# Kernel optimization log

Hardware: AMD Instinct MI355X
Metric: run time of the kernel (lower is better)

Reference implementation:

```python
import jax, jax.numpy as jnp
import numpy as np

N_EMBD = 1024
N_HEAD = 16
HEAD_DIM = N_EMBD // N_HEAD
D_FF = 4 * N_EMBD
B, T = 2, 2048


def setup_inputs() -> dict:
    key = jax.random.key(0)
    ks = jax.random.split(key, 16)
    s = 0.02
    d = {
        'x': jax.random.normal(ks[0], (B, T, N_EMBD), jnp.float32),
        'ln1_g': jnp.ones((N_EMBD,), jnp.float32),
        'ln1_b': jnp.zeros((N_EMBD,), jnp.float32),
        'Wq': jax.random.normal(ks[1], (N_EMBD, N_EMBD), jnp.float32) * s,
        'bq': jnp.zeros((N_EMBD,), jnp.float32),
        'Wk': jax.random.normal(ks[2], (N_EMBD, N_EMBD), jnp.float32) * s,
        'bk': jnp.zeros((N_EMBD,), jnp.float32),
        'Wv': jax.random.normal(ks[3], (N_EMBD, N_EMBD), jnp.float32) * s,
        'bv': jnp.zeros((N_EMBD,), jnp.float32),
        'Wo': jax.random.normal(ks[4], (N_EMBD, N_EMBD), jnp.float32) * s,
        'bo': jnp.zeros((N_EMBD,), jnp.float32),
        'ln2_g': jnp.ones((N_EMBD,), jnp.float32),
        'ln2_b': jnp.zeros((N_EMBD,), jnp.float32),
        'W1': jax.random.normal(ks[5], (N_EMBD, D_FF), jnp.float32) * s,
        'b1': jnp.zeros((D_FF,), jnp.float32),
        'W2': jax.random.normal(ks[6], (D_FF, N_EMBD), jnp.float32) * s,
        'b2': jnp.zeros((N_EMBD,), jnp.float32),
    }
    return d


def _layernorm(x, g, b, eps=1e-5):
    mu = jnp.mean(x, axis=-1, keepdims=True)
    var = jnp.var(x, axis=-1, keepdims=True)
    return (x - mu) * jax.lax.rsqrt(var + eps) * g + b


def _attention(x, Wq, bq, Wk, bk, Wv, bv, Wo, bo):
    b, t, c = x.shape
    q = (x @ Wq + bq).reshape(b, t, N_HEAD, HEAD_DIM).transpose(0, 2, 1, 3)
    k = (x @ Wk + bk).reshape(b, t, N_HEAD, HEAD_DIM).transpose(0, 2, 1, 3)
    v = (x @ Wv + bv).reshape(b, t, N_HEAD, HEAD_DIM).transpose(0, 2, 1, 3)
    att = jnp.einsum('bhqd,bhkd->bhqk', q, k) / jnp.sqrt(jnp.float32(HEAD_DIM))
    causal = jnp.tril(jnp.ones((t, t), bool))
    att = jnp.where(causal[None, None], att, -jnp.inf)
    att = jax.nn.softmax(att, axis=-1)
    y = jnp.einsum('bhqk,bhkd->bhqd', att, v)
    y = y.transpose(0, 2, 1, 3).reshape(b, t, c)
    return y @ Wo + bo


def reference(x, ln1_g, ln1_b, Wq, bq, Wk, bk, Wv, bv, Wo, bo, ln2_g, ln2_b, W1, b1, W2, b2):
    x = x + _attention(_layernorm(x, ln1_g, ln1_b), Wq, bq, Wk, bk, Wv, bv, Wo, bo)
    h = _layernorm(x, ln2_g, ln2_b)
    h = jax.nn.gelu(h @ W1 + b1, approximate=False) @ W2 + b2
    return x + h
```

## Files before the change

### kernel.cpp

```cpp
#include <hip/hip_runtime.h>
#include <hip/hip_bf16.h>

typedef __hip_bfloat16 bf16;
using bf16x8 = __attribute__((ext_vector_type(8))) short;
using f32x4  = __attribute__((ext_vector_type(4))) float;
using f32x16 = __attribute__((ext_vector_type(16))) float;
using u32x4  = __attribute__((ext_vector_type(4))) unsigned int;

#define TSEQ 2048
#define NH   16
#define HD   64
#define NC   1024
#define DFF  4096
#define NROWS 4096

__device__ __forceinline__ float b2f(short s) {
  unsigned int u = ((unsigned int)(unsigned short)s) << 16;
  return __builtin_bit_cast(float, u);
}

__device__ __forceinline__ unsigned cvtpk(float a, float b) {
  unsigned r;
  asm("v_cvt_pk_bf16_f32 %0, %1, %2" : "=v"(r) : "v"(a), "v"(b));
  return r;
}

__device__ __forceinline__ void pl32swap(unsigned &d, unsigned &s) {
  asm("v_permlane32_swap_b32 %0, %1" : "+v"(d), "+v"(s));
}

__device__ __forceinline__ float gelu_f(float x) {
  float u = 0.7978845608028654f * fmaf(0.044715f * x, x * x, x);
  float e = __expf(2.0f * u);
  float t = 1.0f - 2.0f / (e + 1.0f);
  return 0.5f * x * (1.0f + t);
}

__global__ __launch_bounds__(256)
void ln_cast_kernel(const float* __restrict__ x, const float* __restrict__ g,
                    const float* __restrict__ b, bf16* __restrict__ out) {
  int row = blockIdx.x, tid = threadIdx.x;
  const float4 v = ((const float4*)(x + (size_t)row * NC))[tid];
  float s  = v.x + v.y + v.z + v.w;
  float s2 = v.x*v.x + v.y*v.y + v.z*v.z + v.w*v.w;
#pragma unroll
  for (int m = 1; m < 64; m <<= 1) { s += __shfl_xor(s, m); s2 += __shfl_xor(s2, m); }
  __shared__ float rs[4], rs2[4];
  if ((tid & 63) == 0) { rs[tid >> 6] = s; rs2[tid >> 6] = s2; }
  __syncthreads();
  s  = rs[0] + rs[1] + rs[2] + rs[3];
  s2 = rs2[0] + rs2[1] + rs2[2] + rs2[3];
  float mu   = s * (1.0f / NC);
  float var  = s2 * (1.0f / NC) - mu * mu;
  float rstd = rsqrtf(var + 1e-5f);
  const float4 gv = ((const float4*)g)[tid];
  const float4 bv = ((const float4*)b)[tid];
  bf16* o = out + (size_t)row * NC + tid * 4;
  o[0] = __float2bfloat16((v.x - mu) * rstd * gv.x + bv.x);
  o[1] = __float2bfloat16((v.y - mu) * rstd * gv.y + bv.y);
  o[2] = __float2bfloat16((v.z - mu) * rstd * gv.z + bv.z);
  o[3] = __float2bfloat16((v.w - mu) * rstd * gv.w + bv.w);
}

__global__ __launch_bounds__(256)
void wo_ln_kernel(const float* __restrict__ x, const float* __restrict__ bo,
                  const bf16* __restrict__ P, const float* __restrict__ g,
                  const float* __restrict__ bln, float* __restrict__ x2,
                  bf16* __restrict__ xn2) {
  int row = blockIdx.x, tid = threadIdx.x;
  size_t base = (size_t)row * NC + tid * 4;
  const float4 xv = *(const float4*)(x + base);
  const float4 bv = ((const float4*)bo)[tid];
  short4 p0 = *(const short4*)((const short*)P + base);
  short4 p1 = *(const short4*)((const short*)P + (size_t)NROWS * NC + base);
  float v0 = xv.x + bv.x + b2f(p0.x) + b2f(p1.x);
  float v1 = xv.y + bv.y + b2f(p0.y) + b2f(p1.y);
  float v2 = xv.z + bv.z + b2f(p0.z) + b2f(p1.z);
  float v3 = xv.w + bv.w + b2f(p0.w) + b2f(p1.w);
  float4 ov = {v0, v1, v2, v3};
  *(float4*)(x2 + base) = ov;
  float s  = v0 + v1 + v2 + v3;
  float s2 = v0*v0 + v1*v1 + v2*v2 + v3*v3;
#pragma unroll
  for (int m = 1; m < 64; m <<= 1) { s += __shfl_xor(s, m); s2 += __shfl_xor(s2, m); }
  __shared__ float rs[4], rs2[4];
  if ((tid & 63) == 0) { rs[tid >> 6] = s; rs2[tid >> 6] = s2; }
  __syncthreads();
  s  = rs[0] + rs[1] + rs[2] + rs[3];
  s2 = rs2[0] + rs2[1] + rs2[2] + rs2[3];
  float mu   = s * (1.0f / NC);
  float var  = s2 * (1.0f / NC) - mu * mu;
  float rstd = rsqrtf(var + 1e-5f);
  const float4 gv = ((const float4*)g)[tid];
  const float4 lv = ((const float4*)bln)[tid];
  bf16* o = xn2 + base;
  o[0] = __float2bfloat16((v0 - mu) * rstd * gv.x + lv.x);
  o[1] = __float2bfloat16((v1 - mu) * rstd * gv.y + lv.y);
  o[2] = __float2bfloat16((v2 - mu) * rstd * gv.z + lv.z);
  o[3] = __float2bfloat16((v3 - mu) * rstd * gv.w + lv.w);
}

__global__ __launch_bounds__(256)
void w2_final_kernel(const float* __restrict__ x2, const float* __restrict__ b2,
                     const bf16* __restrict__ P, float* __restrict__ out) {
  int row = blockIdx.x, tid = threadIdx.x;
  size_t base = (size_t)row * NC + tid * 4;
  const float4 xv = *(const float4*)(x2 + base);
  const float4 bv = ((const float4*)b2)[tid];
  float a0 = xv.x + bv.x, a1 = xv.y + bv.y, a2 = xv.z + bv.z, a3 = xv.w + bv.w;
#pragma unroll
  for (int z = 0; z < 4; ++z) {
    short4 p = *(const short4*)((const short*)P + (size_t)z * NROWS * NC + base);
    a0 += b2f(p.x); a1 += b2f(p.y); a2 += b2f(p.z); a3 += b2f(p.w);
  }
  float4 ov = {a0, a1, a2, a3};
  *(float4*)(out + base) = ov;
}

__global__ __launch_bounds__(256)
void transpose_all_kernel(const float* __restrict__ Wq, const float* __restrict__ Wk,
                          const float* __restrict__ Wv, const float* __restrict__ Wo,
                          const float* __restrict__ W1, const float* __restrict__ W2,
                          bf16* __restrict__ WqkvoT, bf16* __restrict__ W1T,
                          bf16* __restrict__ W2T) {
  int bid = blockIdx.x;
  const float* W; bf16* Wt; int K, N, nx, tile;
  if (bid < 4096) {
    int z = bid >> 10; tile = bid & 1023;
    W = (z == 0) ? Wq : (z == 1) ? Wk : (z == 2) ? Wv : Wo;
    Wt = WqkvoT + (size_t)z * NC * NC; K = NC; N = NC; nx = 32;
  } else if (bid < 8192) {
    tile = bid - 4096; W = W1; Wt = W1T; K = NC; N = DFF; nx = 128;
  } else {
    tile = bid - 8192; W = W2; Wt = W2T; K = DFF; N = NC; nx = 32;
  }
  int n0 = (tile % nx) * 32, k0 = (tile / nx) * 32;
  __shared__ float t[32][33];
  int tx = threadIdx.x, ty = threadIdx.y;
#pragma unroll
  for (int i = 0; i < 4; ++i)
    t[ty + i * 8][tx] = W[(size_t)(k0 + ty + i * 8) * N + n0 + tx];
  __syncthreads();
#pragma unroll
  for (int i = 0; i < 4; ++i)
    Wt[(size_t)(n0 + ty + i * 8) * K + k0 + tx] = __float2bfloat16(t[tx][ty + i * 8]);
}

#define MODE_GELU 4
#define MODE_QKV  5
#define MODE_PART 6

template <int MODE>
__global__ __launch_bounds__(512, 2)
void gemm256(const bf16* __restrict__ A, const bf16* __restrict__ Bt,
             const float* __restrict__ bias, const float* __restrict__ bias2,
             const float* __restrict__ bias3,
             void* __restrict__ outp, void* __restrict__ out2, void* __restrict__ out3,
             int M, int N, int K, int KS) {
  __shared__ bf16 lds[32768];
  int tid  = threadIdx.x;
  int w    = tid >> 6;
  int lane = tid & 63;
  int l31  = lane & 31;
  int kb   = lane >> 5;
  int wm   = w >> 2, wn = w & 3;

  int gN = gridDim.x, gM = gridDim.y;
  int pid = blockIdx.y * gN + blockIdx.x;
  int npg = 4 * gN;
  int gid = pid / npg;
  int fm  = gid * 4;
  int gsz = min(gM - fm, 4);
  int bm = (fm + (pid % gsz)) * 256;
  int bn = ((pid % npg) / gsz) * 256;
  int k_beg = blockIdx.z * KS;

  int c = lane & 3;
  int q = lane >> 2;
  const bf16* gA = A  + (size_t)(bm + w * 32 + q) * K + k_beg + c * 8;
  const bf16* gB = Bt + (size_t)(bn + w * 32 + q) * K + k_beg + c * 8;
  int wr = (w * 2 + (c >> 1)) * 512 + ((c & 1) * 32 + q) * 8;

  bf16x8 ra0, ra1, rb0, rb1;
  ra0 = *(const bf16x8*)(gA);
  ra1 = *(const bf16x8*)(gA + (size_t)16 * K);
  rb0 = *(const bf16x8*)(gB);
  rb1 = *(const bf16x8*)(gB + (size_t)16 * K);

  f32x16 acc[4][2];
#pragma unroll
  for (int mi = 0; mi < 4; ++mi)
#pragma unroll
    for (int ni = 0; ni < 2; ++ni)
#pragma unroll
      for (int r = 0; r < 16; ++r) acc[mi][ni][r] = 0.f;

  int NT = KS >> 5;
  for (int t = 0; t < NT; ++t) {
    bf16* dA = &lds[(t & 1) * 8192];
    bf16* dB = &lds[16384 + (t & 1) * 8192];
    *(bf16x8*)(dA + wr)       = ra0;
    *(bf16x8*)(dA + wr + 128) = ra1;
    *(bf16x8*)(dB + wr)       = rb0;
    *(bf16x8*)(dB + wr + 128) = rb1;
    if (t + 1 < NT) {
      size_t ko = (size_t)(t + 1) * 32;
      ra0 = *(const bf16x8*)(gA + ko);
      ra1 = *(const bf16x8*)(gA + ko + (size_t)16 * K);
      rb0 = *(const bf16x8*)(gB + ko);
      rb1 = *(const bf16x8*)(gB + ko + (size_t)16 * K);
    }
    __builtin_amdgcn_sched_barrier(0);
    asm volatile("s_waitcnt lgkmcnt(0)" ::: "memory");
    __builtin_amdgcn_s_barrier();
    __builtin_amdgcn_sched_barrier(0);

    const bf16* bufA = &lds[(t & 1) * 8192];
    const bf16* bufB = &lds[16384 + (t & 1) * 8192];
    bf16x8 af[2][4], bfr[2][2];
#pragma unroll
    for (int ks = 0; ks < 2; ++ks) {
#pragma unroll
      for (int mi = 0; mi < 4; ++mi)
        af[ks][mi] = *(const bf16x8*)&bufA[((wm * 4 + mi) * 2 + ks) * 512 + lane * 8];
#pragma unroll
      for (int ni = 0; ni < 2; ++ni)
        bfr[ks][ni] = *(const bf16x8*)&bufB[((wn * 2 + ni) * 2 + ks) * 512 + lane * 8];
    }
    __builtin_amdgcn_s_setprio(1);
#pragma unroll
    for (int ks = 0; ks < 2; ++ks)
#pragma unroll
      for (int mi = 0; mi < 4; ++mi)
#pragma unroll
        for (int ni = 0; ni < 2; ++ni)
          acc[mi][ni] = __builtin_amdgcn_mfma_f32_32x32x16_bf16(af[ks][mi], bfr[ks][ni], acc[mi][ni], 0, 0, 0);
    __builtin_amdgcn_s_setprio(0);
  }

  if (MODE == MODE_PART) {
    bf16* dst = (bf16*)outp + (size_t)blockIdx.z * M * N;
#pragma unroll
    for (int mi = 0; mi < 4; ++mi)
#pragma unroll
      for (int ni = 0; ni < 2; ++ni) {
        int col = bn + wn * 64 + ni * 32 + l31;
#pragma unroll
        for (int reg = 0; reg < 16; ++reg) {
          int row = bm + wm * 128 + mi * 32 + (reg & 3) + 8 * (reg >> 2) + 4 * kb;
          dst[(size_t)row * N + col] = __float2bfloat16(acc[mi][ni][reg]);
        }
      }
  } else if (MODE == MODE_GELU) {
    float bcol[2];
#pragma unroll
    for (int ni = 0; ni < 2; ++ni) bcol[ni] = bias[bn + wn * 64 + ni * 32 + l31];
#pragma unroll
    for (int mi = 0; mi < 4; ++mi)
#pragma unroll
      for (int ni = 0; ni < 2; ++ni) {
        int col = bn + wn * 64 + ni * 32 + l31;
#pragma unroll
        for (int reg = 0; reg < 16; ++reg) {
          int row = bm + wm * 128 + mi * 32 + (reg & 3) + 8 * (reg >> 2) + 4 * kb;
          ((bf16*)outp)[(size_t)row * N + col] =
              __float2bfloat16(gelu_f(acc[mi][ni][reg] + bcol[ni]));
        }
      }
  } else {
    int seg = bn >> 10;
    int c1b = (bn & (NC - 1)) + wn * 64;
    const float* bp = (seg == 0) ? bias : (seg == 1) ? bias2 : bias3;
    float bcol[2]; int hh[2], dd[2];
#pragma unroll
    for (int ni = 0; ni < 2; ++ni) {
      int c1 = c1b + ni * 32 + l31;
      bcol[ni] = bp[c1]; hh[ni] = c1 >> 6; dd[ni] = c1 & (HD - 1);
    }
    if (seg == 0) {
      bf16* dst = (bf16*)outp;
#pragma unroll
      for (int mi = 0; mi < 4; ++mi)
#pragma unroll
        for (int reg = 0; reg < 16; ++reg) {
          int row = bm + wm * 128 + mi * 32 + (reg & 3) + 8 * (reg >> 2) + 4 * kb;
          int bbi = row >> 11, t = row & (TSEQ - 1);
#pragma unroll
          for (int ni = 0; ni < 2; ++ni)
            dst[((size_t)(bbi * NH + hh[ni]) * TSEQ + t) * HD + dd[ni]] =
                __float2bfloat16(acc[mi][ni][reg] + bcol[ni]);
        }
    } else if (seg == 1) {
      bf16* dst = (bf16*)out2;
#pragma unroll
      for (int mi = 0; mi < 4; ++mi)
#pragma unroll
        for (int reg = 0; reg < 16; ++reg) {
          int row = bm + wm * 128 + mi * 32 + (reg & 3) + 8 * (reg >> 2) + 4 * kb;
          int bbi = row >> 11, t = row & (TSEQ - 1);
          int kt = t >> 5, lk = t & 31;
#pragma unroll
          for (int ni = 0; ni < 2; ++ni) {
            int d = dd[ni];
            size_t off = ((((size_t)(bbi * NH + hh[ni]) * 64 + kt) * 4 + (d >> 4)) * 64
                          + ((d >> 3) & 1) * 32 + lk) * 8 + (d & 7);
            dst[off] = __float2bfloat16(acc[mi][ni][reg] + bcol[ni]);
          }
        }
    } else {
      bf16* dst = (bf16*)out3;
#pragma unroll
      for (int mi = 0; mi < 4; ++mi)
#pragma unroll
        for (int reg = 0; reg < 16; ++reg) {
          int row = bm + wm * 128 + mi * 32 + (reg & 3) + 8 * (reg >> 2) + 4 * kb;
          int bbi = row >> 11, t = row & (TSEQ - 1);
          int kt = t >> 5, rem = t & 31;
          int ks = rem >> 4, hf = (rem >> 3) & 1, j = rem & 7;
#pragma unroll
          for (int ni = 0; ni < 2; ++ni) {
            int d = dd[ni];
            size_t off = (((((size_t)(bbi * NH + hh[ni]) * 64 + kt) * 2 + (d >> 5)) * 2 + ks) * 64
                          + hf * 32 + (d & 31)) * 8 + j;
            dst[off] = __float2bfloat16(acc[mi][ni][reg] + bcol[ni]);
          }
        }
    }
  }
}

__global__ __launch_bounds__(256)
void attn_kernel(const bf16* __restrict__ q, const bf16* __restrict__ kf,
                 const bf16* __restrict__ vf, bf16* __restrict__ out) {
  int id  = blockIdx.x;
  int xcd = id & 7;
  int t   = id >> 3;
  int bh  = xcd * 4 + (t & 3);
  int u   = t >> 2;
  int qt  = (u < 32) ? (2 * u) : (63 - 2 * (u - 32));
  int b = bh >> 4, h = bh & 15;

  int tid  = threadIdx.x;
  int w    = tid >> 6;
  int lane = tid & 63;
  int l31  = lane & 31;
  int hh   = lane >> 5;
  int h8   = hh * 8;
  int base4 = hh * 4;

  const bf16* qp  = q  + (size_t)(b * NH + h) * TSEQ * HD;
  const bf16* kfb = kf + (size_t)bh * (64 * 4 * 64 * 8);
  const bf16* vfb = vf + (size_t)bh * (64 * 2 * 2 * 64 * 8);

  int q0 = qt * 32;

  bf16x8 qf[4];
#pragma unroll
  for (int ds = 0; ds < 4; ++ds)
    qf[ds] = *(const bf16x8*)(qp + (size_t)(q0 + l31) * HD + ds * 16 + h8);

  f32x16 o0, o1;
#pragma unroll
  for (int r = 0; r < 16; ++r) { o0[r] = 0.f; o1[r] = 0.f; }
  float lacc = 0.f;

  bf16x8 a0, a1, a2, a3;

  auto step = [&](int kt, bool dg) {
    const bf16* vs = vfb + (size_t)kt * 2048 + lane * 8;
    bf16x8 v00 = *(const bf16x8*)(vs);
    bf16x8 v01 = *(const bf16x8*)(vs + 512);
    bf16x8 v10 = *(const bf16x8*)(vs + 1024);
    bf16x8 v11 = *(const bf16x8*)(vs + 1536);
    bf16x8 n0, n1, n2, n3;
    bool pf = !dg && (kt + 4 <= qt);
    if (pf) {
      const bf16* kn = kfb + (size_t)(kt + 4) * 2048 + lane * 8;
      n0 = *(const bf16x8*)(kn);
      n1 = *(const bf16x8*)(kn + 512);
      n2 = *(const bf16x8*)(kn + 1024);
      n3 = *(const bf16x8*)(kn + 1536);
    }

    f32x16 c;
#pragma unroll
    for (int r = 0; r < 16; ++r) c[r] = 0.f;
    c = __builtin_amdgcn_mfma_f32_32x32x16_bf16(a0, qf[0], c, 0, 0, 0);
    c = __builtin_amdgcn_mfma_f32_32x32x16_bf16(a1, qf[1], c, 0, 0, 0);
    c = __builtin_amdgcn_mfma_f32_32x32x16_bf16(a2, qf[2], c, 0, 0, 0);
    c = __builtin_amdgcn_mfma_f32_32x32x16_bf16(a3, qf[3], c, 0, 0, 0);

    float p[16];
    float ls = 0.f;
#pragma unroll
    for (int r = 0; r < 16; ++r) {
      float pv = exp2f(fmaf(c[r], 0.18033688011112042f, -11.541560327111707f));
      if (dg) {
        int krr = (r & 3) + 8 * (r >> 2) + base4;
        pv = (krr <= l31) ? pv : 0.f;
      }
      p[r] = pv;
      ls += pv;
    }
    lacc += ls;

    unsigned A0 = cvtpk(p[0],  p[1]),  C0 = cvtpk(p[4],  p[5]);
    unsigned B0 = cvtpk(p[2],  p[3]),  D0 = cvtpk(p[6],  p[7]);
    pl32swap(A0, C0); pl32swap(B0, D0);
    unsigned A1 = cvtpk(p[8],  p[9]),  C1 = cvtpk(p[12], p[13]);
    unsigned B1 = cvtpk(p[10], p[11]), D1 = cvtpk(p[14], p[15]);
    pl32swap(A1, C1); pl32swap(B1, D1);
    u32x4 w0v = {A0, B0, C0, D0};
    u32x4 w1v = {A1, B1, C1, D1};
    bf16x8 pa0 = __builtin_bit_cast(bf16x8, w0v);
    bf16x8 pa1 = __builtin_bit_cast(bf16x8, w1v);

    o0 = __builtin_amdgcn_mfma_f32_32x32x16_bf16(pa0, v00, o0, 0, 0, 0);
    o0 = __builtin_amdgcn_mfma_f32_32x32x16_bf16(pa1, v01, o0, 0, 0, 0);
    o1 = __builtin_amdgcn_mfma_f32_32x32x16_bf16(pa0, v10, o1, 0, 0, 0);
    o1 = __builtin_amdgcn_mfma_f32_32x32x16_bf16(pa1, v11, o1, 0, 0, 0);

    if (pf) { a0 = n0; a1 = n1; a2 = n2; a3 = n3; }
  };

  if (w <= qt) {
    const bf16* ka = kfb + (size_t)w * 2048 + lane * 8;
    a0 = *(const bf16x8*)(ka);
    a1 = *(const bf16x8*)(ka + 512);
    a2 = *(const bf16x8*)(ka + 1024);
    a3 = *(const bf16x8*)(ka + 1536);
    int diag = (w == (qt & 3)) ? 1 : 0;
    int T = ((qt - w) >> 2) + 1 - diag;
    int kt = w;
    for (int i = 0; i < T; ++i, kt += 4) step(kt, false);
    if (diag) step(qt, true);
  }

  __shared__ float red[2][64][33];
  auto dump = [&](int slot) {
    float* d = &red[slot][lane][0];
#pragma unroll
    for (int r = 0; r < 16; ++r) { d[r] = o0[r]; d[16 + r] = o1[r]; }
    d[32] = lacc;
  };
  auto gather = [&](int slot) {
    const float* s = &red[slot][lane][0];
#pragma unroll
    for (int r = 0; r < 16; ++r) { o0[r] += s[r]; o1[r] += s[16 + r]; }
    lacc += s[32];
  };
  if (w >= 2) dump(w - 2);
  __syncthreads();
  if (w < 2) gather(w);
  __syncthreads();
  if (w == 1) dump(0);
  __syncthreads();
  if (w == 0) {
    gather(0);
    float ltot = lacc + __shfl_xor(lacc, 32);
    float linv = 1.0f / ltot;
#pragma unroll
    for (int r = 0; r < 16; ++r) {
      int qoff = (r & 3) + 8 * (r >> 2) + base4;
      float sc = __shfl(linv, qoff);
      size_t ob = ((size_t)(b * TSEQ + q0 + qoff)) * NC + h * HD + l31;
      out[ob]      = __float2bfloat16(o0[r] * sc);
      out[ob + 32] = __float2bfloat16(o1[r] * sc);
    }
  }
}

extern "C" void kernel_launch(void* const* d_in, const int* in_sizes, int n_in,
                              void* d_out, int out_size, void* d_ws, size_t ws_size,
                              hipStream_t stream) {
  const float* x     = (const float*)d_in[0];
  const float* ln1_g = (const float*)d_in[1];
  const float* ln1_b = (const float*)d_in[2];
  const float* Wq    = (const float*)d_in[3];
  const float* bq    = (const float*)d_in[4];
  const float* Wk    = (const float*)d_in[5];
  const float* bk    = (const float*)d_in[6];
  const float* Wv    = (const float*)d_in[7];
  const float* bv    = (const float*)d_in[8];
  const float* Wo    = (const float*)d_in[9];
  const float* bo    = (const float*)d_in[10];
  const float* ln2_g = (const float*)d_in[11];
  const float* ln2_b = (const float*)d_in[12];
  const float* W1    = (const float*)d_in[13];
  const float* b1    = (const float*)d_in[14];
  const float* W2    = (const float*)d_in[15];
  const float* b2    = (const float*)d_in[16];

  char* ws = (char*)d_ws;
  const size_t MB = 1u << 20;
  bf16* WqkvT = (bf16*)(ws + 0 * MB);
  bf16* W1T  = (bf16*)(ws + 8 * MB);
  bf16* W2T  = (bf16*)(ws + 16 * MB);
  bf16* xn1  = (bf16*)(ws + 24 * MB);
  bf16* qb   = (bf16*)(ws + 32 * MB);
  bf16* kfB  = (bf16*)(ws + 40 * MB);
  bf16* vfB  = (bf16*)(ws + 48 * MB);
  bf16* att  = (bf16*)(ws + 56 * MB);
  float* x2  = (float*)(ws + 64 * MB);
  bf16* xn2  = (bf16*)(ws + 80 * MB);
  bf16* h1   = (bf16*)(ws + 88 * MB);
  bf16* woP  = (bf16*)(ws + 88 * MB);
  bf16* w2P  = (bf16*)(ws + 32 * MB);
  bf16* WoT  = WqkvT + 3 * (size_t)NC * NC;

  transpose_all_kernel<<<12288, dim3(32, 8), 0, stream>>>(
      Wq, Wk, Wv, Wo, W1, W2, WqkvT, W1T, W2T);

  ln_cast_kernel<<<NROWS, 256, 0, stream>>>(x, ln1_g, ln1_b, xn1);

  gemm256<MODE_QKV><<<dim3(12, 16, 1), 512, 0, stream>>>(
      xn1, WqkvT, bq, bk, bv, qb, kfB, vfB, NROWS, 3 * NC, NC, NC);

  attn_kernel<<<2048, 256, 0, stream>>>(qb, kfB, vfB, att);

  gemm256<MODE_PART><<<dim3(4, 16, 2), 512, 0, stream>>>(
      att, WoT, nullptr, nullptr, nullptr, woP, nullptr, nullptr, NROWS, NC, NC, NC / 2);

  wo_ln_kernel<<<NROWS, 256, 0, stream>>>(x, bo, woP, ln2_g, ln2_b, x2, xn2);

  gemm256<MODE_GELU><<<dim3(16, 16, 1), 512, 0, stream>>>(
      xn2, W1T, b1, nullptr, nullptr, h1, nullptr, nullptr, NROWS, DFF, NC, NC);

  gemm256<MODE_PART><<<dim3(4, 16, 4), 512, 0, stream>>>(
      h1, W2T, nullptr, nullptr, nullptr, w2P, nullptr, nullptr, NROWS, NC, DFF, DFF / 4);

  w2_final_kernel<<<NROWS, 256, 0, stream>>>(x2, b2, w2P, (float*)d_out);
}
```

Measured before the change: 339.1 us.

## Prepack weights in MFMA fragment order and load B directly to registers

The weight transpose kernel now writes weights in a pre-swizzled MFMA-fragment layout. The GEMM then loads each wave's B fragments straight from global memory into registers, skipping the LDS staging for B and halving LDS use. A-tile LDS writes and reads get an XOR swizzle to reduce bank conflicts. In exchange, B tiles are no longer shared through LDS, so every wave (wm 0 and 1) fetches its own B fragments from global/L2, which raises global traffic. B data is also now loaded at most one iteration ahead.

```diff
diff --git a/kernel.cpp b/kernel.cpp
--- a/kernel.cpp
+++ b/kernel.cpp
@@ -141,9 +141,14 @@
   for (int i = 0; i < 4; ++i)
     t[ty + i * 8][tx] = W[(size_t)(k0 + ty + i * 8) * N + n0 + tx];
   __syncthreads();
-#pragma unroll
-  for (int i = 0; i < 4; ++i)
-    Wt[(size_t)(n0 + ty + i * 8) * K + k0 + tx] = __float2bfloat16(t[tx][ty + i * 8]);
+  int NKT = K >> 5;
+#pragma unroll
+  for (int i = 0; i < 4; ++i) {
+    int n = n0 + ty + i * 8, k = k0 + tx;
+    size_t off = ((((size_t)((n >> 5) * NKT + (k >> 5)) * 2 + ((k >> 4) & 1)) * 64)
+                  + ((k >> 3) & 1) * 32 + (n & 31)) * 8 + (k & 7);
+    Wt[off] = __float2bfloat16(t[tx][ty + i * 8]);
+  }
 }
 
 #define MODE_GELU 4
@@ -152,12 +157,12 @@
 
 template <int MODE>
 __global__ __launch_bounds__(512, 2)
-void gemm256(const bf16* __restrict__ A, const bf16* __restrict__ Bt,
+void gemm256(const bf16* __restrict__ A, const bf16* __restrict__ Bf,
              const float* __restrict__ bias, const float* __restrict__ bias2,
              const float* __restrict__ bias3,
              void* __restrict__ outp, void* __restrict__ out2, void* __restrict__ out3,
              int M, int N, int K, int KS) {
-  __shared__ bf16 lds[32768];
+  __shared__ bf16 lds[16384];
   int tid  = threadIdx.x;
   int w    = tid >> 6;
   int lane = tid & 63;
@@ -177,15 +182,27 @@
 
   int c = lane & 3;
   int q = lane >> 2;
-  const bf16* gA = A  + (size_t)(bm + w * 32 + q) * K + k_beg + c * 8;
-  const bf16* gB = Bt + (size_t)(bn + w * 32 + q) * K + k_beg + c * 8;
-  int wr = (w * 2 + (c >> 1)) * 512 + ((c & 1) * 32 + q) * 8;
-
-  bf16x8 ra0, ra1, rb0, rb1;
-  ra0 = *(const bf16x8*)(gA);
-  ra1 = *(const bf16x8*)(gA + (size_t)16 * K);
-  rb0 = *(const bf16x8*)(gB);
-  rb1 = *(const bf16x8*)(gB + (size_t)16 * K);
+  const bf16* gA = A + (size_t)(bm + w * 32 + q) * K + k_beg + c * 8;
+  int wrE = (((w * 2 + (c >> 1)) * 512 + ((c & 1) * 32 + q) * 8))
+            ^ (((c & 1) << 4) | ((c >> 1) << 5));
+  int lrE = (lane * 8) ^ ((lane >> 5) << 4);
+  int lrO = lrE ^ 32;
+
+  int NKT = K >> 5;
+  int K0  = k_beg >> 5;
+  const bf16* bp[2];
+#pragma unroll
+  for (int ni = 0; ni < 2; ++ni) {
+    int g = (bn >> 5) + wn * 2 + ni;
+    bp[ni] = Bf + ((size_t)(g * NKT + K0) * 2) * 512 + lane * 8;
+  }
+
+  bf16x8 ra0 = *(const bf16x8*)(gA);
+  bf16x8 ra1 = *(const bf16x8*)(gA + (size_t)16 * K);
+  bf16x8 bf00 = *(const bf16x8*)(bp[0]);
+  bf16x8 bf01 = *(const bf16x8*)(bp[1]);
+  bf16x8 bf10 = *(const bf16x8*)(bp[0] + 512);
+  bf16x8 bf11 = *(const bf16x8*)(bp[1] + 512);
 
   f32x16 acc[4][2];
 #pragma unroll
@@ -198,17 +215,18 @@
   int NT = KS >> 5;
   for (int t = 0; t < NT; ++t) {
     bf16* dA = &lds[(t & 1) * 8192];
-    bf16* dB = &lds[16384 + (t & 1) * 8192];
-    *(bf16x8*)(dA + wr)       = ra0;
-    *(bf16x8*)(dA + wr + 128) = ra1;
-    *(bf16x8*)(dB + wr)       = rb0;
-    *(bf16x8*)(dB + wr + 128) = rb1;
+    *(bf16x8*)(dA + wrE)       = ra0;
+    *(bf16x8*)(dA + wrE + 128) = ra1;
+    bf16x8 nb00, nb01, nb10, nb11;
     if (t + 1 < NT) {
       size_t ko = (size_t)(t + 1) * 32;
       ra0 = *(const bf16x8*)(gA + ko);
       ra1 = *(const bf16x8*)(gA + ko + (size_t)16 * K);
-      rb0 = *(const bf16x8*)(gB + ko);
-      rb1 = *(const bf16x8*)(gB + ko + (size_t)16 * K);
+      size_t bo_ = (size_t)(t + 1) * 1024;
+      nb00 = *(const bf16x8*)(bp[0] + bo_);
+      nb01 = *(const bf16x8*)(bp[1] + bo_);
+      nb10 = *(const bf16x8*)(bp[0] + bo_ + 512);
+      nb11 = *(const bf16x8*)(bp[1] + bo_ + 512);
     }
     __builtin_amdgcn_sched_barrier(0);
     asm volatile("s_waitcnt lgkmcnt(0)" ::: "memory");
@@ -216,26 +234,27 @@
     __builtin_amdgcn_sched_barrier(0);
 
     const bf16* bufA = &lds[(t & 1) * 8192];
-    const bf16* bufB = &lds[16384 + (t & 1) * 8192];
-    bf16x8 af[2][4], bfr[2][2];
-#pragma unroll
-    for (int ks = 0; ks < 2; ++ks) {
-#pragma unroll
-      for (int mi = 0; mi < 4; ++mi)
-        af[ks][mi] = *(const bf16x8*)&bufA[((wm * 4 + mi) * 2 + ks) * 512 + lane * 8];
-#pragma unroll
-      for (int ni = 0; ni < 2; ++ni)
-        bfr[ks][ni] = *(const bf16x8*)&bufB[((wn * 2 + ni) * 2 + ks) * 512 + lane * 8];
-    }
+    bf16x8 af[2][4];
+#pragma unroll
+    for (int ks = 0; ks < 2; ++ks)
+#pragma unroll
+      for (int mi = 0; mi < 4; ++mi) {
+        int g2 = (wm * 4 + mi) * 2 + ks;
+        af[ks][mi] = *(const bf16x8*)&bufA[g2 * 512 + ((g2 & 1) ? lrO : lrE)];
+      }
     __builtin_amdgcn_s_setprio(1);
 #pragma unroll
-    for (int ks = 0; ks < 2; ++ks)
-#pragma unroll
-      for (int mi = 0; mi < 4; ++mi)
-#pragma unroll
-        for (int ni = 0; ni < 2; ++ni)
-          acc[mi][ni] = __builtin_amdgcn_mfma_f32_32x32x16_bf16(af[ks][mi], bfr[ks][ni], acc[mi][ni], 0, 0, 0);
+    for (int mi = 0; mi < 4; ++mi) {
+      acc[mi][0] = __builtin_amdgcn_mfma_f32_32x32x16_bf16(af[0][mi], bf00, acc[mi][0], 0, 0, 0);
+      acc[mi][1] = __builtin_amdgcn_mfma_f32_32x32x16_bf16(af[0][mi], bf01, acc[mi][1], 0, 0, 0);
+    }
+#pragma unroll
+    for (int mi = 0; mi < 4; ++mi) {
+      acc[mi][0] = __builtin_amdgcn_mfma_f32_32x32x16_bf16(af[1][mi], bf10, acc[mi][0], 0, 0, 0);
+      acc[mi][1] = __builtin_amdgcn_mfma_f32_32x32x16_bf16(af[1][mi], bf11, acc[mi][1], 0, 0, 0);
+    }
     __builtin_amdgcn_s_setprio(0);
+    if (t + 1 < NT) { bf00 = nb00; bf01 = nb01; bf10 = nb10; bf11 = nb11; }
   }
 
   if (MODE == MODE_PART) {
@@ -270,12 +289,12 @@
   } else {
     int seg = bn >> 10;
     int c1b = (bn & (NC - 1)) + wn * 64;
-    const float* bp = (seg == 0) ? bias : (seg == 1) ? bias2 : bias3;
+    const float* bpb = (seg == 0) ? bias : (seg == 1) ? bias2 : bias3;
     float bcol[2]; int hh[2], dd[2];
 #pragma unroll
     for (int ni = 0; ni < 2; ++ni) {
       int c1 = c1b + ni * 32 + l31;
-      bcol[ni] = bp[c1]; hh[ni] = c1 >> 6; dd[ni] = c1 & (HD - 1);
+      bcol[ni] = bpb[c1]; hh[ni] = c1 >> 6; dd[ni] = c1 & (HD - 1);
     }
     if (seg == 0) {
       bf16* dst = (bf16*)outp;
```

New measurement: 333.7 us. Within noise of the previous version (-1.6%).
